# Performance work log

Measured on AMD Instinct MI355X. Metric: run time of the kernel, lower is better.

## Reference

```python
import jax, jax.numpy as jnp
import numpy as np

N_A, N_G, D, H = 100000, 25000, 128, 4
E_B, E_O, E_R, E_P = 400000, 100000, 200000, 200000
BN_INV = float(1.0 / np.sqrt(1.0 + 1e-5))  # eval-mode BatchNorm1d, running mean 0 / var 1


def setup_inputs():
    key = jax.random.key(0)
    ks = iter(jax.random.split(key, 64))
    nrm = lambda shape, s=0.05: jax.random.normal(next(ks), shape, jnp.float32) * s
    ri = lambda n, hi: jax.random.randint(next(ks), (n,), 0, hi, jnp.int32)
    inp = dict(
        x_atom=nrm((N_A, D), 1.0), x_group=nrm((N_G, D), 1.0),
        ef_bond=nrm((E_B, D), 1.0), ef_overlap=nrm((E_O, D), 1.0),
        bond_src=ri(E_B, N_A), bond_dst=ri(E_B, N_A),
        ov_src=ri(E_O, N_G), ov_dst=ri(E_O, N_G),
        ref_src=ri(E_R, N_G), ref_dst=ri(E_R, N_A),
        pool_src=ri(E_P, N_A), pool_dst=ri(E_P, N_G),
    )
    # two GINE convs (bond 'b', overlap 'o'): eps + MLP Linear(D,2D)->BN->ReLU->Linear(2D,D)
    for pre in ('b', 'o'):
        inp[pre + '_eps'] = jnp.zeros((1,), jnp.float32)
        inp[pre + '_W1'] = nrm((D, 2 * D)); inp[pre + '_b1'] = jnp.zeros((2 * D,), jnp.float32)
        inp[pre + '_g1'] = jnp.ones((2 * D,), jnp.float32); inp[pre + '_be1'] = jnp.zeros((2 * D,), jnp.float32)
        inp[pre + '_W2'] = nrm((2 * D, D)); inp[pre + '_b2'] = jnp.zeros((D,), jnp.float32)
    # two ModifiedGATConvs (refine 'r', pool 'p'): GATConv + Flatten->BN->ReLU->Linear
    for pre in ('r', 'p'):
        inp[pre + '_Wfc'] = nrm((D, H * D)); inp[pre + '_al'] = nrm((H, D)); inp[pre + '_ar'] = nrm((H, D))
        inp[pre + '_Wres'] = nrm((D, H * D)); inp[pre + '_bias'] = jnp.zeros((H * D,), jnp.float32)
        inp[pre + '_g'] = jnp.ones((H * D,), jnp.float32); inp[pre + '_b'] = jnp.zeros((H * D,), jnp.float32)
        inp[pre + '_Wout'] = nrm((H * D, D)); inp[pre + '_bout'] = jnp.zeros((D,), jnp.float32)
    return inp


def _gine(x_src, x_dst, efeat, src, dst, n_dst, eps, W1, b1, g1, be1, W2, b2):
    m = jax.nn.relu(x_src[src] + efeat)                       # [E, D] message: relu(h_src + e)
    neigh = jax.ops.segment_sum(m, dst, num_segments=n_dst)   # [Nd, D] sum-reduce
    h = (1.0 + eps) * x_dst + neigh
    h = h @ W1 + b1
    h = jax.nn.relu(g1 * (h * BN_INV) + be1)                  # eval BN
    return h @ W2 + b2


def _gat(x_src, x_dst, src, dst, n_dst, Wfc, al, ar, Wres, bias, g, b, Wout, bout):
    hs = (x_src @ Wfc).reshape(-1, H, D)                      # [Ns, H, D]
    hd = (x_dst @ Wfc).reshape(-1, H, D)
    el = jnp.sum(hs * al, axis=-1)                            # [Ns, H]
    er = jnp.sum(hd * ar, axis=-1)                            # [Nd, H]
    e = jax.nn.leaky_relu(el[src] + er[dst], 0.2)             # [E, H]
    emax = jax.ops.segment_max(e, dst, num_segments=n_dst)    # per-dst softmax (stable)
    ex = jnp.exp(e - emax[dst])
    den = jax.ops.segment_sum(ex, dst, num_segments=n_dst)
    a = ex / jnp.maximum(den[dst], 1e-9)                      # [E, H]
    rst = jax.ops.segment_sum(a[:, :, None] * hs[src], dst, num_segments=n_dst)  # [Nd, H, D]
    rst = rst + (x_dst @ Wres).reshape(-1, H, D) + bias.reshape(H, D)            # residual + bias
    flat = rst.reshape(-1, H * D)                             # Flatten
    h = jax.nn.relu(g * (flat * BN_INV) + b)                  # eval BN -> ReLU
    return h @ Wout + bout


def reference(x_atom, x_group, ef_bond, ef_overlap, bond_src, bond_dst, ov_src, ov_dst, ref_src, ref_dst, pool_src, pool_dst, b_eps, b_W1, b_b1, b_g1, b_be1, b_W2, b_b2, o_eps, o_W1, o_b1, o_g1, o_be1, o_W2, o_b2, r_Wfc, r_al, r_ar, r_Wres, r_bias, r_g, r_b, r_Wout, r_bout, p_Wfc, p_al, p_ar, p_Wres, p_bias, p_g, p_b, p_Wout, p_bout):
    # HeteroGraphConv with default 'sum' cross-relation aggregation per dst node type
    out_atom = _gine(x_atom, x_atom, ef_bond, bond_src, bond_dst, N_A, b_eps, b_W1, b_b1, b_g1, b_be1, b_W2, b_b2)
    out_atom = out_atom + _gat(x_group, x_atom, ref_src, ref_dst, N_A, r_Wfc, r_al, r_ar, r_Wres, r_bias, r_g, r_b, r_Wout, r_bout)
    out_group = _gine(x_group, x_group, ef_overlap, ov_src, ov_dst, N_G, o_eps, o_W1, o_b1, o_g1, o_be1, o_W2, o_b2)
    out_group = out_group + _gat(x_atom, x_group, pool_src, pool_dst, N_G, p_Wfc, p_al, p_ar, p_Wres, p_bias, p_g, p_b, p_Wout, p_bout)
    return jnp.concatenate([out_atom, out_group], axis=0)     # [N_A + N_G, D]
```

## Files before the change

### kernel.cpp

```cpp
#include <hip/hip_runtime.h>
#include <hip/hip_bf16.h>

#define N_A 100000
#define N_G 25000
#define DD 128
#define E_B 400000
#define E_O 100000
#define E_R 200000
#define E_P 200000
#define EALL 900000
#define NSLOT 250000
#define STRIDE 64

static constexpr float BN_INV_C = 0.99999500003749969f;

typedef __attribute__((ext_vector_type(8))) short bf16x8;
typedef __attribute__((ext_vector_type(4))) float f32x4;

__device__ __forceinline__ unsigned short f2bf(float f) {
    unsigned u = __float_as_uint(f);
    unsigned r = (u + 0x7FFFu + ((u >> 16) & 1u)) >> 16;
    return (unsigned short)r;
}
__device__ __forceinline__ float bf2f(unsigned short s) {
    return __uint_as_float(((unsigned)s) << 16);
}
__device__ __forceinline__ float lrelu(float v) { return v > 0.f ? v : 0.2f * v; }

__global__ void k_xcast_all(const float* __restrict__ xa, const float* __restrict__ xg,
                            unsigned short* __restrict__ xab, unsigned short* __restrict__ xgb) {
    int t = blockIdx.x * blockDim.x + threadIdx.x;
    if (t < N_A * 32) {
        float4 v = *(const float4*)(xa + (size_t)t * 4);
        ushort4 o; o.x = f2bf(v.x); o.y = f2bf(v.y); o.z = f2bf(v.z); o.w = f2bf(v.w);
        *(ushort4*)(xab + (size_t)t * 4) = o;
    } else {
        int t2 = t - N_A * 32;
        if (t2 >= N_G * 32) return;
        float4 v = *(const float4*)(xg + (size_t)t2 * 4);
        ushort4 o; o.x = f2bf(v.x); o.y = f2bf(v.y); o.z = f2bf(v.z); o.w = f2bf(v.w);
        *(ushort4*)(xgb + (size_t)t2 * 4) = o;
    }
}

struct WcSeg { const float* src; unsigned short* dst; int K; int N; int ldk; int off; };
struct WcArgs { WcSeg s[10]; };

__global__ void k_wcast_all(WcArgs a) {
    WcSeg sg = a.s[blockIdx.y];
    int t = blockIdx.x * blockDim.x + threadIdx.x;
    if (t >= sg.K * sg.N) return;
    int n = t % sg.N, k = t / sg.N;
    sg.dst[(size_t)n * sg.ldk + sg.off + k] = f2bf(sg.src[t]);
}

__global__ void k_war_all(const float* __restrict__ rWfc, const float* __restrict__ ral,
                          const float* __restrict__ rar, const float* __restrict__ pWfc,
                          const float* __restrict__ pal, const float* __restrict__ par,
                          float* __restrict__ wv) {
    int bsel = blockIdx.x;
    const float* W = bsel < 2 ? rWfc : pWfc;
    const float* vec = bsel == 0 ? ral : bsel == 1 ? rar : bsel == 2 ? pal : par;
    float* o = wv + bsel * 512;
    int t = threadIdx.x;
    int k = t >> 2, h = t & 3;
    const float* wr = W + (size_t)k * 512 + h * 128;
    const float* av = vec + h * 128;
    float s = 0.f;
    for (int d = 0; d < 128; ++d) s += wr[d] * av[d];
    o[t] = s;
}

__global__ void k_adj_fill(const int* __restrict__ bs, const int* __restrict__ bd,
                           const int* __restrict__ os, const int* __restrict__ od,
                           const int* __restrict__ rs, const int* __restrict__ rd,
                           const int* __restrict__ ps, const int* __restrict__ pd,
                           int* __restrict__ deg, uint2* __restrict__ adj,
                           int* __restrict__ heads, int* __restrict__ nxt) {
    int t = blockIdx.x * blockDim.x + threadIdx.x;
    int e, base, go; const int* S; const int* D;
    if (t < E_B) { e = t; S = bs; D = bd; base = 0; go = 0; }
    else if (t < E_B + E_O) { e = t - E_B; S = os; D = od; base = 100000; go = E_B; }
    else if (t < E_B + E_O + E_R) { e = t - (E_B + E_O); S = rs; D = rd; base = 125000; go = E_B + E_O; }
    else if (t < EALL) { e = t - (E_B + E_O + E_R); S = ps; D = pd; base = 225000; go = E_B + E_O + E_R; }
    else return;
    int d = D[e], s = S[e];
    int ns = base + d;
    int pos = atomicAdd(&deg[ns], 1);
    if (pos < STRIDE) adj[(size_t)ns * STRIDE + pos] = make_uint2((unsigned)e, (unsigned)s);
    else nxt[go + e] = atomicExch(&heads[ns], e);
}

__global__ __launch_bounds__(256) void k_gine_gather_all(
    const unsigned short* __restrict__ xAb, const unsigned short* __restrict__ xGb,
    const float* __restrict__ efB, const float* __restrict__ efO,
    const int* __restrict__ bsrc, const int* __restrict__ osrc,
    const int* __restrict__ deg, const uint2* __restrict__ adj,
    const int* __restrict__ heads, const int* __restrict__ nxt,
    const float* __restrict__ beps, const float* __restrict__ oeps,
    unsigned short* __restrict__ h0A, unsigned short* __restrict__ h0G) {
    int wid = threadIdx.x >> 6, lane = threadIdx.x & 63;
    int n = blockIdx.x * 4 + wid;
    __shared__ uint2 gl[4][STRIDE];
    const unsigned short* xs; const unsigned short* xdrow; const float* ef;
    const int* esrc; const int* nx; float ep; unsigned short* outp; int nn, base, go;
    if (n < N_A) {
        nn = n; xs = xAb; xdrow = xAb + (size_t)n * DD; ef = efB; esrc = bsrc;
        base = 0; go = 0; ep = 1.0f + beps[0]; outp = h0A + (size_t)n * DD;
    } else {
        nn = n - N_A; xs = xGb; xdrow = xGb + (size_t)nn * DD; ef = efO; esrc = osrc;
        base = 100000; go = E_B; ep = 1.0f + oeps[0]; outp = h0G + (size_t)nn * DD;
    }
    nx = nxt + go;
    int d = deg[base + nn];
    int cb = min(d, STRIDE);
    if (lane < cb) gl[wid][lane] = adj[(size_t)(base + nn) * STRIDE + lane];
    __syncthreads();
    float2 acc = make_float2(0.f, 0.f);
    for (int i = 0; i < cb; ++i) {
        uint2 es = gl[wid][i];
        unsigned xa = *(const unsigned*)(xs + (size_t)es.y * DD + lane * 2);
        float2 ev = *(const float2*)(ef + (size_t)es.x * DD + lane * 2);
        acc.x += fmaxf(bf2f((unsigned short)(xa & 0xffff)) + ev.x, 0.f);
        acc.y += fmaxf(bf2f((unsigned short)(xa >> 16)) + ev.y, 0.f);
    }
    if (d > STRIDE) {
        for (int e = heads[base + nn]; e >= 0; e = nx[e]) {
            int s = esrc[e];
            unsigned xa = *(const unsigned*)(xs + (size_t)s * DD + lane * 2);
            float2 ev = *(const float2*)(ef + (size_t)e * DD + lane * 2);
            acc.x += fmaxf(bf2f((unsigned short)(xa & 0xffff)) + ev.x, 0.f);
            acc.y += fmaxf(bf2f((unsigned short)(xa >> 16)) + ev.y, 0.f);
        }
    }
    unsigned xd = *(const unsigned*)(xdrow + lane * 2);
    float rx = ep * bf2f((unsigned short)(xd & 0xffff)) + acc.x;
    float ry = ep * bf2f((unsigned short)(xd >> 16)) + acc.y;
    *(unsigned*)(outp + lane * 2) = (unsigned)f2bf(rx) | ((unsigned)f2bf(ry) << 16);
}

__global__ void k_el_all(const unsigned short* __restrict__ xAb,
                         const unsigned short* __restrict__ xGb,
                         const float* __restrict__ wv,
                         float* __restrict__ elR, float* __restrict__ elP) {
    int t = blockIdx.x * blockDim.x + threadIdx.x;
    const unsigned short* xr; const float* wvp; float* op; int idx;
    if (t < N_G * 4) {
        idx = t; xr = xGb + (size_t)(t >> 2) * DD; wvp = wv; op = elR;
    } else {
        int t2 = t - N_G * 4;
        if (t2 >= N_A * 4) return;
        idx = t2; xr = xAb + (size_t)(t2 >> 2) * DD; wvp = wv + 1024; op = elP;
    }
    int h = idx & 3;
    float s = 0.f;
#pragma unroll
    for (int k = 0; k < DD; k += 8) {
        uint4 w = *(const uint4*)(xr + k);
        unsigned wa[4] = {w.x, w.y, w.z, w.w};
#pragma unroll
        for (int q = 0; q < 4; ++q) {
            s += bf2f((unsigned short)(wa[q] & 0xffff)) * wvp[(k + q * 2) * 4 + h];
            s += bf2f((unsigned short)(wa[q] >> 16)) * wvp[(k + q * 2 + 1) * 4 + h];
        }
    }
    op[idx] = s;
}

__global__ __launch_bounds__(256) void k_att_gather_all(
    const unsigned short* __restrict__ xAb, const unsigned short* __restrict__ xGb,
    const float* __restrict__ elR, const float* __restrict__ elP,
    const float* __restrict__ wv,
    const int* __restrict__ rsrc, const int* __restrict__ psrc,
    const int* __restrict__ deg, const uint2* __restrict__ adj,
    const int* __restrict__ heads, const int* __restrict__ nxt,
    unsigned short* __restrict__ A2r, unsigned short* __restrict__ A2p) {
    int wid = threadIdx.x >> 6, lane = threadIdx.x & 63;
    int n = blockIdx.x * 4 + wid;
    __shared__ int sl[4][STRIDE];
    __shared__ float sa[4][4][STRIDE];
    const unsigned short* xs; const unsigned short* xdrow; const float* el;
    const float* wvr; const int* esrc; const int* nx;
    unsigned short* A2; int nn, base, go;
    if (n < N_A) {
        nn = n; xs = xGb; xdrow = xAb + (size_t)n * DD; el = elR; wvr = wv + 512;
        esrc = rsrc; base = 125000; go = E_B + E_O;
        A2 = A2r + (size_t)n * 512;
    } else {
        nn = n - N_A; xs = xAb; xdrow = xGb + (size_t)nn * DD; el = elP; wvr = wv + 1536;
        esrc = psrc; base = 225000; go = E_B + E_O + E_R;
        A2 = A2p + (size_t)nn * 512;
    }
    nx = nxt + go;
    int d = deg[base + nn];
    int cb = min(d, STRIDE);
    if (lane < cb) sl[wid][lane] = (int)adj[(size_t)(base + nn) * STRIDE + lane].y;
    __syncthreads();
    unsigned xd = *(const unsigned*)(xdrow + lane * 2);
    float xd0 = bf2f((unsigned short)(xd & 0xffff));
    float xd1 = bf2f((unsigned short)(xd >> 16));
    float er[4];
#pragma unroll
    for (int h = 0; h < 4; ++h)
        er[h] = xd0 * wvr[(2 * lane) * 4 + h] + xd1 * wvr[(2 * lane + 1) * 4 + h];
#pragma unroll
    for (int m = 1; m < 64; m <<= 1) {
#pragma unroll
        for (int h = 0; h < 4; ++h) er[h] += __shfl_xor(er[h], m, 64);
    }
    float mx[4] = {-1e30f, -1e30f, -1e30f, -1e30f};
    float lv[4] = {0.f, 0.f, 0.f, 0.f};
    if (lane < cb) {
        int s = sl[wid][lane];
        float4 e4 = *(const float4*)(el + (size_t)s * 4);
        lv[0] = lrelu(e4.x + er[0]); lv[1] = lrelu(e4.y + er[1]);
        lv[2] = lrelu(e4.z + er[2]); lv[3] = lrelu(e4.w + er[3]);
#pragma unroll
        for (int h = 0; h < 4; ++h) mx[h] = lv[h];
    }
#pragma unroll
    for (int m = 1; m < 64; m <<= 1) {
#pragma unroll
        for (int h = 0; h < 4; ++h) mx[h] = fmaxf(mx[h], __shfl_xor(mx[h], m, 64));
    }
    if (d > STRIDE) {
        for (int e = heads[base + nn]; e >= 0; e = nx[e]) {
            int s = esrc[e];
            float4 e4 = *(const float4*)(el + (size_t)s * 4);
            mx[0] = fmaxf(mx[0], lrelu(e4.x + er[0]));
            mx[1] = fmaxf(mx[1], lrelu(e4.y + er[1]));
            mx[2] = fmaxf(mx[2], lrelu(e4.z + er[2]));
            mx[3] = fmaxf(mx[3], lrelu(e4.w + er[3]));
        }
    }
    float den[4] = {0.f, 0.f, 0.f, 0.f};
    if (lane < cb) {
#pragma unroll
        for (int h = 0; h < 4; ++h) {
            float v = __expf(lv[h] - mx[h]);
            sa[wid][h][lane] = v;
            den[h] = v;
        }
    }
#pragma unroll
    for (int m = 1; m < 64; m <<= 1) {
#pragma unroll
        for (int h = 0; h < 4; ++h) den[h] += __shfl_xor(den[h], m, 64);
    }
    if (d > STRIDE) {
        for (int e = heads[base + nn]; e >= 0; e = nx[e]) {
            int s = esrc[e];
            float4 e4 = *(const float4*)(el + (size_t)s * 4);
            den[0] += __expf(lrelu(e4.x + er[0]) - mx[0]);
            den[1] += __expf(lrelu(e4.y + er[1]) - mx[1]);
            den[2] += __expf(lrelu(e4.z + er[2]) - mx[2]);
            den[3] += __expf(lrelu(e4.w + er[3]) - mx[3]);
        }
    }
    float inv[4];
#pragma unroll
    for (int h = 0; h < 4; ++h) inv[h] = 1.f / fmaxf(den[h], 1e-9f);
    __syncthreads();
    float acc[4][2] = {};
    for (int i = 0; i < cb; ++i) {
        int s = sl[wid][i];
        float a0 = sa[wid][0][i] * inv[0];
        float a1 = sa[wid][1][i] * inv[1];
        float a2 = sa[wid][2][i] * inv[2];
        float a3 = sa[wid][3][i] * inv[3];
        unsigned xw = *(const unsigned*)(xs + (size_t)s * DD + lane * 2);
        float x0 = bf2f((unsigned short)(xw & 0xffff));
        float x1 = bf2f((unsigned short)(xw >> 16));
        acc[0][0] += a0 * x0; acc[0][1] += a0 * x1;
        acc[1][0] += a1 * x0; acc[1][1] += a1 * x1;
        acc[2][0] += a2 * x0; acc[2][1] += a2 * x1;
        acc[3][0] += a3 * x0; acc[3][1] += a3 * x1;
    }
    if (d > STRIDE) {
        for (int e = heads[base + nn]; e >= 0; e = nx[e]) {
            int s = esrc[e];
            float4 e4 = *(const float4*)(el + (size_t)s * 4);
            unsigned xw = *(const unsigned*)(xs + (size_t)s * DD + lane * 2);
            float x0 = bf2f((unsigned short)(xw & 0xffff));
            float x1 = bf2f((unsigned short)(xw >> 16));
            float a0 = __expf(lrelu(e4.x + er[0]) - mx[0]) * inv[0];
            float a1 = __expf(lrelu(e4.y + er[1]) - mx[1]) * inv[1];
            float a2 = __expf(lrelu(e4.z + er[2]) - mx[2]) * inv[2];
            float a3 = __expf(lrelu(e4.w + er[3]) - mx[3]) * inv[3];
            acc[0][0] += a0 * x0; acc[0][1] += a0 * x1;
            acc[1][0] += a1 * x0; acc[1][1] += a1 * x1;
            acc[2][0] += a2 * x0; acc[2][1] += a2 * x1;
            acc[3][0] += a3 * x0; acc[3][1] += a3 * x1;
        }
    }
#pragma unroll
    for (int h = 0; h < 4; ++h) {
        unsigned o = (unsigned)f2bf(acc[h][0]) | ((unsigned)f2bf(acc[h][1]) << 16);
        *(unsigned*)(A2 + h * 128 + lane * 2) = o;
    }
}

#define LDKP 40
template <int EPI, int OUTBF, int GATK>
__global__ __launch_bounds__(256) void k_gemm_bf(
    const unsigned short* __restrict__ A, const unsigned short* __restrict__ Bt,
    void* __restrict__ C, int M, int N, int K,
    const float* __restrict__ bias, const float* __restrict__ g,
    const float* __restrict__ be, const unsigned short* __restrict__ addbf,
    const unsigned short* __restrict__ Axd) {
    __shared__ unsigned short As[128 * LDKP];
    __shared__ unsigned short Bs[128 * LDKP];
    int tid = threadIdx.x;
    int wave = tid >> 6, lane = tid & 63;
    int wr = wave >> 1, wc = wave & 1;
    int row0 = blockIdx.y * 128, col0 = blockIdx.x * 128;
    int l16 = lane & 15, khalf = (lane >> 4) * 8;
    f32x4 acc[4][4] = {};
    int r_0 = tid >> 2, ko_0 = (tid & 3) * 8;
    int r_1 = (tid + 256) >> 2, ko_1 = ((tid + 256) & 3) * 8;
    for (int k0 = 0; k0 < K; k0 += 32) {
        __syncthreads();
        {
            int kk = k0 + ko_0;
            int ra = min(row0 + r_0, M - 1);
            uint4 va;
            if (GATK) va = (kk < 128) ? *(const uint4*)(A + (size_t)ra * 512 + col0 + kk)
                                      : *(const uint4*)(Axd + (size_t)ra * 128 + (kk - 128));
            else va = *(const uint4*)(A + (size_t)ra * K + kk);
            *(uint4*)(&As[r_0 * LDKP + ko_0]) = va;
            uint4 vb = *(const uint4*)(Bt + (size_t)(col0 + r_0) * K + kk);
            *(uint4*)(&Bs[r_0 * LDKP + ko_0]) = vb;
            kk = k0 + ko_1;
            ra = min(row0 + r_1, M - 1);
            if (GATK) va = (kk < 128) ? *(const uint4*)(A + (size_t)ra * 512 + col0 + kk)
                                      : *(const uint4*)(Axd + (size_t)ra * 128 + (kk - 128));
            else va = *(const uint4*)(A + (size_t)ra * K + kk);
            *(uint4*)(&As[r_1 * LDKP + ko_1]) = va;
            vb = *(const uint4*)(Bt + (size_t)(col0 + r_1) * K + kk);
            *(uint4*)(&Bs[r_1 * LDKP + ko_1]) = vb;
        }
        __syncthreads();
        bf16x8 af[4], bfr[4];
#pragma unroll
        for (int i = 0; i < 4; ++i)
            af[i] = *(const bf16x8*)(&As[(wr * 64 + i * 16 + l16) * LDKP + khalf]);
#pragma unroll
        for (int j = 0; j < 4; ++j)
            bfr[j] = *(const bf16x8*)(&Bs[(wc * 64 + j * 16 + l16) * LDKP + khalf]);
#pragma unroll
        for (int i = 0; i < 4; ++i)
#pragma unroll
            for (int j = 0; j < 4; ++j)
                acc[i][j] = __builtin_amdgcn_mfma_f32_16x16x32_bf16(af[i], bfr[j], acc[i][j], 0, 0, 0);
    }
    int rq = (lane >> 4) * 4;
#pragma unroll
    for (int i = 0; i < 4; ++i) {
#pragma unroll
        for (int reg = 0; reg < 4; ++reg) {
            int r = row0 + wr * 64 + i * 16 + rq + reg;
            if (r >= M) continue;
#pragma unroll
            for (int j = 0; j < 4; ++j) {
                int c = col0 + wc * 64 + j * 16 + l16;
                float v = acc[i][j][reg];
                size_t idx = (size_t)r * N + c;
                v += bias[c];
                if (EPI == 2) {
                    v = g[c] * (v * BN_INV_C) + be[c];
                    v = fmaxf(v, 0.f);
                }
                if (EPI == 3) {
                    ((float*)C)[idx] = v + bf2f(addbf[idx]);
                } else if (OUTBF) {
                    ((unsigned short*)C)[idx] = f2bf(v);
                } else {
                    ((float*)C)[idx] = v;
                }
            }
        }
    }
}

extern "C" void kernel_launch(void* const* d_in, const int* in_sizes, int n_in,
                              void* d_out, int out_size, void* d_ws, size_t ws_size,
                              hipStream_t stream) {
    const float* x_atom = (const float*)d_in[0];
    const float* x_group = (const float*)d_in[1];
    const float* ef_bond = (const float*)d_in[2];
    const float* ef_ov = (const float*)d_in[3];
    const int* bond_src = (const int*)d_in[4];
    const int* bond_dst = (const int*)d_in[5];
    const int* ov_src = (const int*)d_in[6];
    const int* ov_dst = (const int*)d_in[7];
    const int* ref_src = (const int*)d_in[8];
    const int* ref_dst = (const int*)d_in[9];
    const int* pool_src = (const int*)d_in[10];
    const int* pool_dst = (const int*)d_in[11];
    const float* b_eps = (const float*)d_in[12];
    const float* b_W1 = (const float*)d_in[13];
    const float* b_b1 = (const float*)d_in[14];
    const float* b_g1 = (const float*)d_in[15];
    const float* b_be1 = (const float*)d_in[16];
    const float* b_W2 = (const float*)d_in[17];
    const float* b_b2 = (const float*)d_in[18];
    const float* o_eps = (const float*)d_in[19];
    const float* o_W1 = (const float*)d_in[20];
    const float* o_b1 = (const float*)d_in[21];
    const float* o_g1 = (const float*)d_in[22];
    const float* o_be1 = (const float*)d_in[23];
    const float* o_W2 = (const float*)d_in[24];
    const float* o_b2 = (const float*)d_in[25];
    const float* r_Wfc = (const float*)d_in[26];
    const float* r_al = (const float*)d_in[27];
    const float* r_ar = (const float*)d_in[28];
    const float* r_Wres = (const float*)d_in[29];
    const float* r_bias = (const float*)d_in[30];
    const float* r_g = (const float*)d_in[31];
    const float* r_b = (const float*)d_in[32];
    const float* r_Wout = (const float*)d_in[33];
    const float* r_bout = (const float*)d_in[34];
    const float* p_Wfc = (const float*)d_in[35];
    const float* p_al = (const float*)d_in[36];
    const float* p_ar = (const float*)d_in[37];
    const float* p_Wres = (const float*)d_in[38];
    const float* p_bias = (const float*)d_in[39];
    const float* p_g = (const float*)d_in[40];
    const float* p_b = (const float*)d_in[41];
    const float* p_Wout = (const float*)d_in[42];
    const float* p_bout = (const float*)d_in[43];

    float* out = (float*)d_out;
    char* wsb = (char*)d_ws;
    unsigned short* xAb = (unsigned short*)(wsb + 0);
    unsigned short* xGb = (unsigned short*)(wsb + 26000000);
    unsigned short* WtB1 = (unsigned short*)(wsb + 33000000);
    unsigned short* WtB2 = WtB1 + 32768;
    unsigned short* WtO1 = WtB2 + 32768;
    unsigned short* WtO2 = WtO1 + 32768;
    unsigned short* WtR  = WtO2 + 32768;
    unsigned short* WtRo = WtR + 131072;
    unsigned short* WtP  = WtRo + 65536;
    unsigned short* WtPo = WtP + 131072;
    float* wv   = (float*)(wsb + 34100000);
    float* elR  = (float*)(wsb + 34200000);
    float* elP  = (float*)(wsb + 34600000);
    int* heads  = (int*)(wsb + 36300000);
    int* nxt    = (int*)(wsb + 37400000);
    unsigned short* h0A = (unsigned short*)(wsb + 41100000);
    unsigned short* h0G = (unsigned short*)(wsb + 66800000);
    unsigned short* R4  = (unsigned short*)(wsb + 73300000);
    unsigned short* G1a = (unsigned short*)(wsb + 124600000);
    unsigned short* G1g = (unsigned short*)(wsb + 150300000);
    unsigned short* A2r = (unsigned short*)(wsb + 156800000);
    unsigned short* A2p = (unsigned short*)(wsb + 259300000);
    unsigned short* R3r = (unsigned short*)(wsb + 285000000);
    unsigned short* R3p = (unsigned short*)(wsb + 387500000);
    uint2* adj  = (uint2*)(wsb + 414000000);
    int* deg    = (int*)(wsb + 543000000);

    k_xcast_all<<<((N_A + N_G) * 32 + 255) / 256, 256, 0, stream>>>(x_atom, x_group, xAb, xGb);
    WcArgs wa;
    wa.s[0] = {b_W1, WtB1, 128, 256, 128, 0};
    wa.s[1] = {b_W2, WtB2, 256, 128, 256, 0};
    wa.s[2] = {o_W1, WtO1, 128, 256, 128, 0};
    wa.s[3] = {o_W2, WtO2, 256, 128, 256, 0};
    wa.s[4] = {r_Wfc, WtR, 128, 512, 256, 0};
    wa.s[5] = {r_Wres, WtR, 128, 512, 256, 128};
    wa.s[6] = {r_Wout, WtRo, 512, 128, 512, 0};
    wa.s[7] = {p_Wfc, WtP, 128, 512, 256, 0};
    wa.s[8] = {p_Wres, WtP, 128, 512, 256, 128};
    wa.s[9] = {p_Wout, WtPo, 512, 128, 512, 0};
    k_wcast_all<<<dim3(256, 10), 256, 0, stream>>>(wa);
    k_war_all<<<4, 512, 0, stream>>>(r_Wfc, r_al, r_ar, p_Wfc, p_al, p_ar, wv);
    hipMemsetAsync(deg, 0, NSLOT * 4, stream);
    hipMemsetAsync(heads, 0xFF, NSLOT * 4, stream);
    k_adj_fill<<<(EALL + 255) / 256, 256, 0, stream>>>(
        bond_src, bond_dst, ov_src, ov_dst, ref_src, ref_dst, pool_src, pool_dst,
        deg, adj, heads, nxt);
    k_gine_gather_all<<<31250, 256, 0, stream>>>(xAb, xGb, ef_bond, ef_ov, bond_src, ov_src,
                                                 deg, adj, heads, nxt, b_eps, o_eps, h0A, h0G);
    k_gemm_bf<2, 1, 0><<<dim3(2, 782), 256, 0, stream>>>(h0A, WtB1, R4, N_A, 256, 128, b_b1, b_g1, b_be1, nullptr, nullptr);
    k_gemm_bf<1, 1, 0><<<dim3(1, 782), 256, 0, stream>>>(R4, WtB2, G1a, N_A, 128, 256, b_b2, nullptr, nullptr, nullptr, nullptr);
    k_gemm_bf<2, 1, 0><<<dim3(2, 196), 256, 0, stream>>>(h0G, WtO1, R4, N_G, 256, 128, o_b1, o_g1, o_be1, nullptr, nullptr);
    k_gemm_bf<1, 1, 0><<<dim3(1, 196), 256, 0, stream>>>(R4, WtO2, G1g, N_G, 128, 256, o_b2, nullptr, nullptr, nullptr, nullptr);
    k_el_all<<<((N_G + N_A) * 4 + 255) / 256, 256, 0, stream>>>(xAb, xGb, wv, elR, elP);
    k_att_gather_all<<<31250, 256, 0, stream>>>(xAb, xGb, elR, elP, wv, ref_src, pool_src,
                                                deg, adj, heads, nxt, A2r, A2p);
    k_gemm_bf<2, 1, 1><<<dim3(4, 782), 256, 0, stream>>>(A2r, WtR, R3r, N_A, 512, 256, r_bias, r_g, r_b, nullptr, xAb);
    k_gemm_bf<2, 1, 1><<<dim3(4, 196), 256, 0, stream>>>(A2p, WtP, R3p, N_G, 512, 256, p_bias, p_g, p_b, nullptr, xGb);
    k_gemm_bf<3, 0, 0><<<dim3(1, 782), 256, 0, stream>>>(R3r, WtRo, out, N_A, 128, 512, r_bout, nullptr, nullptr, G1a, nullptr);
    k_gemm_bf<3, 0, 0><<<dim3(1, 196), 256, 0, stream>>>(R3p, WtPo, out + (size_t)N_A * DD, N_G, 128, 512, p_bout, nullptr, nullptr, G1g, nullptr);
}
```

Measured before the change: 607.1 us.

## Precompute GAT edge softmax exponentials with atomic denominators in separate edge kernel

Computes per-node right logits alongside left logits, then adds an edge-parallel kernel that evaluates exp(leaky_relu) per edge and head and accumulates softmax denominators with atomics. The attention gather kernel then reads precomputed exponentials and denominators, which removes the per-node max/denominator shuffle reductions and the repeated overflow-list passes. The max subtraction is dropped, so the softmax is no longer numerically stabilised and could overflow for large logits. It also adds atomics, one more launch and an extra memset.

```diff
diff --git a/kernel.cpp b/kernel.cpp
--- a/kernel.cpp
+++ b/kernel.cpp
@@ -139,138 +139,103 @@
     *(unsigned*)(outp + lane * 2) = (unsigned)f2bf(rx) | ((unsigned)f2bf(ry) << 16);
 }
 
-__global__ void k_el_all(const unsigned short* __restrict__ xAb,
-                         const unsigned short* __restrict__ xGb,
-                         const float* __restrict__ wv,
-                         float* __restrict__ elR, float* __restrict__ elP) {
+__global__ void k_logit_all(const unsigned short* __restrict__ xAb,
+                            const unsigned short* __restrict__ xGb,
+                            const float* __restrict__ wv,
+                            float* __restrict__ elR, float* __restrict__ elP,
+                            float* __restrict__ erR, float* __restrict__ erP) {
     int t = blockIdx.x * blockDim.x + threadIdx.x;
-    const unsigned short* xr; const float* wvp; float* op; int idx;
-    if (t < N_G * 4) {
-        idx = t; xr = xGb + (size_t)(t >> 2) * DD; wvp = wv; op = elR;
+    const unsigned short* xr; const float* wl; const float* wr_; float* ol; float* orr; int idx;
+    if (t < N_A * 4) {
+        idx = t; xr = xAb + (size_t)(t >> 2) * DD; wl = wv + 1024; wr_ = wv + 512;
+        ol = elP; orr = erR;
     } else {
-        int t2 = t - N_G * 4;
-        if (t2 >= N_A * 4) return;
-        idx = t2; xr = xAb + (size_t)(t2 >> 2) * DD; wvp = wv + 1024; op = elP;
+        int t2 = t - N_A * 4;
+        if (t2 >= N_G * 4) return;
+        idx = t2; xr = xGb + (size_t)(t2 >> 2) * DD; wl = wv; wr_ = wv + 1536;
+        ol = elR; orr = erP;
     }
     int h = idx & 3;
-    float s = 0.f;
+    float sl = 0.f, sr = 0.f;
 #pragma unroll
     for (int k = 0; k < DD; k += 8) {
         uint4 w = *(const uint4*)(xr + k);
         unsigned wa[4] = {w.x, w.y, w.z, w.w};
 #pragma unroll
         for (int q = 0; q < 4; ++q) {
-            s += bf2f((unsigned short)(wa[q] & 0xffff)) * wvp[(k + q * 2) * 4 + h];
-            s += bf2f((unsigned short)(wa[q] >> 16)) * wvp[(k + q * 2 + 1) * 4 + h];
+            float x0 = bf2f((unsigned short)(wa[q] & 0xffff));
+            float x1 = bf2f((unsigned short)(wa[q] >> 16));
+            int k0 = (k + q * 2) * 4 + h, k1 = (k + q * 2 + 1) * 4 + h;
+            sl += x0 * wl[k0] + x1 * wl[k1];
+            sr += x0 * wr_[k0] + x1 * wr_[k1];
         }
     }
-    op[idx] = s;
+    ol[idx] = sl;
+    orr[idx] = sr;
+}
+
+__global__ void k_exp_all(const float* __restrict__ elR, const float* __restrict__ erR,
+                          const float* __restrict__ elP, const float* __restrict__ erP,
+                          const int* __restrict__ rs, const int* __restrict__ rd,
+                          const int* __restrict__ ps, const int* __restrict__ pd,
+                          float* __restrict__ exR, float* __restrict__ exP,
+                          float* __restrict__ denR, float* __restrict__ denP) {
+    int t = blockIdx.x * blockDim.x + threadIdx.x;
+    if (t < E_R * 4) {
+        int e = t >> 2, h = t & 3;
+        float v = lrelu(elR[rs[e] * 4 + h] + erR[rd[e] * 4 + h]);
+        float x = __expf(v);
+        exR[t] = x;
+        atomicAdd(&denR[rd[e] * 4 + h], x);
+    } else {
+        int t2 = t - E_R * 4;
+        if (t2 >= E_P * 4) return;
+        int e = t2 >> 2, h = t2 & 3;
+        float v = lrelu(elP[ps[e] * 4 + h] + erP[pd[e] * 4 + h]);
+        float x = __expf(v);
+        exP[t2] = x;
+        atomicAdd(&denP[pd[e] * 4 + h], x);
+    }
 }
 
 __global__ __launch_bounds__(256) void k_att_gather_all(
     const unsigned short* __restrict__ xAb, const unsigned short* __restrict__ xGb,
-    const float* __restrict__ elR, const float* __restrict__ elP,
-    const float* __restrict__ wv,
+    const float* __restrict__ exR, const float* __restrict__ exP,
+    const float* __restrict__ denR, const float* __restrict__ denP,
     const int* __restrict__ rsrc, const int* __restrict__ psrc,
     const int* __restrict__ deg, const uint2* __restrict__ adj,
     const int* __restrict__ heads, const int* __restrict__ nxt,
     unsigned short* __restrict__ A2r, unsigned short* __restrict__ A2p) {
     int wid = threadIdx.x >> 6, lane = threadIdx.x & 63;
     int n = blockIdx.x * 4 + wid;
-    __shared__ int sl[4][STRIDE];
-    __shared__ float sa[4][4][STRIDE];
-    const unsigned short* xs; const unsigned short* xdrow; const float* el;
-    const float* wvr; const int* esrc; const int* nx;
-    unsigned short* A2; int nn, base, go;
+    __shared__ uint2 gl[4][STRIDE];
+    const unsigned short* xs; const float* ex; const float* den;
+    const int* esrc; const int* nx; unsigned short* A2; int nn, base, go;
     if (n < N_A) {
-        nn = n; xs = xGb; xdrow = xAb + (size_t)n * DD; el = elR; wvr = wv + 512;
-        esrc = rsrc; base = 125000; go = E_B + E_O;
-        A2 = A2r + (size_t)n * 512;
+        nn = n; xs = xGb; ex = exR; den = denR; esrc = rsrc;
+        base = 125000; go = E_B + E_O; A2 = A2r + (size_t)n * 512;
     } else {
-        nn = n - N_A; xs = xAb; xdrow = xGb + (size_t)nn * DD; el = elP; wvr = wv + 1536;
-        esrc = psrc; base = 225000; go = E_B + E_O + E_R;
-        A2 = A2p + (size_t)nn * 512;
+        nn = n - N_A; xs = xAb; ex = exP; den = denP; esrc = psrc;
+        base = 225000; go = E_B + E_O + E_R; A2 = A2p + (size_t)nn * 512;
     }
     nx = nxt + go;
     int d = deg[base + nn];
     int cb = min(d, STRIDE);
-    if (lane < cb) sl[wid][lane] = (int)adj[(size_t)(base + nn) * STRIDE + lane].y;
+    if (lane < cb) gl[wid][lane] = adj[(size_t)(base + nn) * STRIDE + lane];
     __syncthreads();
-    unsigned xd = *(const unsigned*)(xdrow + lane * 2);
-    float xd0 = bf2f((unsigned short)(xd & 0xffff));
-    float xd1 = bf2f((unsigned short)(xd >> 16));
-    float er[4];
-#pragma unroll
-    for (int h = 0; h < 4; ++h)
-        er[h] = xd0 * wvr[(2 * lane) * 4 + h] + xd1 * wvr[(2 * lane + 1) * 4 + h];
-#pragma unroll
-    for (int m = 1; m < 64; m <<= 1) {
-#pragma unroll
-        for (int h = 0; h < 4; ++h) er[h] += __shfl_xor(er[h], m, 64);
-    }
-    float mx[4] = {-1e30f, -1e30f, -1e30f, -1e30f};
-    float lv[4] = {0.f, 0.f, 0.f, 0.f};
-    if (lane < cb) {
-        int s = sl[wid][lane];
-        float4 e4 = *(const float4*)(el + (size_t)s * 4);
-        lv[0] = lrelu(e4.x + er[0]); lv[1] = lrelu(e4.y + er[1]);
-        lv[2] = lrelu(e4.z + er[2]); lv[3] = lrelu(e4.w + er[3]);
-#pragma unroll
-        for (int h = 0; h < 4; ++h) mx[h] = lv[h];
-    }
-#pragma unroll
-    for (int m = 1; m < 64; m <<= 1) {
-#pragma unroll
-        for (int h = 0; h < 4; ++h) mx[h] = fmaxf(mx[h], __shfl_xor(mx[h], m, 64));
-    }
-    if (d > STRIDE) {
-        for (int e = heads[base + nn]; e >= 0; e = nx[e]) {
-            int s = esrc[e];
-            float4 e4 = *(const float4*)(el + (size_t)s * 4);
-            mx[0] = fmaxf(mx[0], lrelu(e4.x + er[0]));
-            mx[1] = fmaxf(mx[1], lrelu(e4.y + er[1]));
-            mx[2] = fmaxf(mx[2], lrelu(e4.z + er[2]));
-            mx[3] = fmaxf(mx[3], lrelu(e4.w + er[3]));
-        }
-    }
-    float den[4] = {0.f, 0.f, 0.f, 0.f};
-    if (lane < cb) {
-#pragma unroll
-        for (int h = 0; h < 4; ++h) {
-            float v = __expf(lv[h] - mx[h]);
-            sa[wid][h][lane] = v;
-            den[h] = v;
-        }
-    }
-#pragma unroll
-    for (int m = 1; m < 64; m <<= 1) {
-#pragma unroll
-        for (int h = 0; h < 4; ++h) den[h] += __shfl_xor(den[h], m, 64);
-    }
-    if (d > STRIDE) {
-        for (int e = heads[base + nn]; e >= 0; e = nx[e]) {
-            int s = esrc[e];
-            float4 e4 = *(const float4*)(el + (size_t)s * 4);
-            den[0] += __expf(lrelu(e4.x + er[0]) - mx[0]);
-            den[1] += __expf(lrelu(e4.y + er[1]) - mx[1]);
-            den[2] += __expf(lrelu(e4.z + er[2]) - mx[2]);
-            den[3] += __expf(lrelu(e4.w + er[3]) - mx[3]);
-        }
-    }
-    float inv[4];
-#pragma unroll
-    for (int h = 0; h < 4; ++h) inv[h] = 1.f / fmaxf(den[h], 1e-9f);
-    __syncthreads();
+    float4 dv = *(const float4*)(den + (size_t)nn * 4);
+    float inv0 = 1.f / fmaxf(dv.x, 1e-9f);
+    float inv1 = 1.f / fmaxf(dv.y, 1e-9f);
+    float inv2 = 1.f / fmaxf(dv.z, 1e-9f);
+    float inv3 = 1.f / fmaxf(dv.w, 1e-9f);
     float acc[4][2] = {};
     for (int i = 0; i < cb; ++i) {
-        int s = sl[wid][i];
-        float a0 = sa[wid][0][i] * inv[0];
-        float a1 = sa[wid][1][i] * inv[1];
-        float a2 = sa[wid][2][i] * inv[2];
-        float a3 = sa[wid][3][i] * inv[3];
-        unsigned xw = *(const unsigned*)(xs + (size_t)s * DD + lane * 2);
+        uint2 es = gl[wid][i];
+        float4 e4 = *(const float4*)(ex + (size_t)es.x * 4);
+        unsigned xw = *(const unsigned*)(xs + (size_t)es.y * DD + lane * 2);
         float x0 = bf2f((unsigned short)(xw & 0xffff));
         float x1 = bf2f((unsigned short)(xw >> 16));
+        float a0 = e4.x * inv0, a1 = e4.y * inv1, a2 = e4.z * inv2, a3 = e4.w * inv3;
         acc[0][0] += a0 * x0; acc[0][1] += a0 * x1;
         acc[1][0] += a1 * x0; acc[1][1] += a1 * x1;
         acc[2][0] += a2 * x0; acc[2][1] += a2 * x1;
@@ -279,14 +244,11 @@
     if (d > STRIDE) {
         for (int e = heads[base + nn]; e >= 0; e = nx[e]) {
             int s = esrc[e];
-            float4 e4 = *(const float4*)(el + (size_t)s * 4);
+            float4 e4 = *(const float4*)(ex + (size_t)e * 4);
             unsigned xw = *(const unsigned*)(xs + (size_t)s * DD + lane * 2);
             float x0 = bf2f((unsigned short)(xw & 0xffff));
             float x1 = bf2f((unsigned short)(xw >> 16));
-            float a0 = __expf(lrelu(e4.x + er[0]) - mx[0]) * inv[0];
-            float a1 = __expf(lrelu(e4.y + er[1]) - mx[1]) * inv[1];
-            float a2 = __expf(lrelu(e4.z + er[2]) - mx[2]) * inv[2];
-            float a3 = __expf(lrelu(e4.w + er[3]) - mx[3]) * inv[3];
+            float a0 = e4.x * inv0, a1 = e4.y * inv1, a2 = e4.z * inv2, a3 = e4.w * inv3;
             acc[0][0] += a0 * x0; acc[0][1] += a0 * x1;
             acc[1][0] += a1 * x0; acc[1][1] += a1 * x1;
             acc[2][0] += a2 * x0; acc[2][1] += a2 * x1;
@@ -443,8 +405,6 @@
     unsigned short* WtP  = WtRo + 65536;
     unsigned short* WtPo = WtP + 131072;
     float* wv   = (float*)(wsb + 34100000);
-    float* elR  = (float*)(wsb + 34200000);
-    float* elP  = (float*)(wsb + 34600000);
     int* heads  = (int*)(wsb + 36300000);
     int* nxt    = (int*)(wsb + 37400000);
     unsigned short* h0A = (unsigned short*)(wsb + 41100000);
@@ -458,6 +418,15 @@
     unsigned short* R3p = (unsigned short*)(wsb + 387500000);
     uint2* adj  = (uint2*)(wsb + 414000000);
     int* deg    = (int*)(wsb + 543000000);
+    float* F    = (float*)(wsb + 544000000);
+    float* elR  = F;
+    float* elP  = F + 100000;
+    float* erR  = F + 500000;
+    float* erP  = F + 900000;
+    float* denR = F + 1000000;
+    float* denP = F + 1400000;
+    float* exR  = F + 1500000;
+    float* exP  = F + 2300000;
 
     k_xcast_all<<<((N_A + N_G) * 32 + 255) / 256, 256, 0, stream>>>(x_atom, x_group, xAb, xGb);
     WcArgs wa;
@@ -475,6 +444,7 @@
     k_war_all<<<4, 512, 0, stream>>>(r_Wfc, r_al, r_ar, p_Wfc, p_al, p_ar, wv);
     hipMemsetAsync(deg, 0, NSLOT * 4, stream);
     hipMemsetAsync(heads, 0xFF, NSLOT * 4, stream);
+    hipMemsetAsync(denR, 0, 500000 * 4, stream);
     k_adj_fill<<<(EALL + 255) / 256, 256, 0, stream>>>(
         bond_src, bond_dst, ov_src, ov_dst, ref_src, ref_dst, pool_src, pool_dst,
         deg, adj, heads, nxt);
@@ -484,8 +454,10 @@
     k_gemm_bf<1, 1, 0><<<dim3(1, 782), 256, 0, stream>>>(R4, WtB2, G1a, N_A, 128, 256, b_b2, nullptr, nullptr, nullptr, nullptr);
     k_gemm_bf<2, 1, 0><<<dim3(2, 196), 256, 0, stream>>>(h0G, WtO1, R4, N_G, 256, 128, o_b1, o_g1, o_be1, nullptr, nullptr);
     k_gemm_bf<1, 1, 0><<<dim3(1, 196), 256, 0, stream>>>(R4, WtO2, G1g, N_G, 128, 256, o_b2, nullptr, nullptr, nullptr, nullptr);
-    k_el_all<<<((N_G + N_A) * 4 + 255) / 256, 256, 0, stream>>>(xAb, xGb, wv, elR, elP);
-    k_att_gather_all<<<31250, 256, 0, stream>>>(xAb, xGb, elR, elP, wv, ref_src, pool_src,
+    k_logit_all<<<((N_A + N_G) * 4 + 255) / 256, 256, 0, stream>>>(xAb, xGb, wv, elR, elP, erR, erP);
+    k_exp_all<<<((E_R + E_P) * 4 + 255) / 256, 256, 0, stream>>>(elR, erR, elP, erP,
+        ref_src, ref_dst, pool_src, pool_dst, exR, exP, denR, denP);
+    k_att_gather_all<<<31250, 256, 0, stream>>>(xAb, xGb, exR, exP, denR, denP, ref_src, pool_src,
                                                 deg, adj, heads, nxt, A2r, A2p);
     k_gemm_bf<2, 1, 1><<<dim3(4, 782), 256, 0, stream>>>(A2r, WtR, R3r, N_A, 512, 256, r_bias, r_g, r_b, nullptr, xAb);
     k_gemm_bf<2, 1, 1><<<dim3(4, 196), 256, 0, stream>>>(A2p, WtP, R3p, N_G, 512, 256, p_bias, p_g, p_b, nullptr, xGb);
```

Result: no change. 596.8 us (-1.7%).
